# Optimization experiments

Hardware: AMD Instinct MI355X
Metric: run time of the kernel (lower is better)

## Reference

```python
import jax, jax.numpy as jnp
import numpy as np

BIG = 5000.0  # knockout sentinel from the original code
LOSS_WEIGHTS = jnp.array([1.0, 1.0, 1.0, 1.0, 1.0])  # [prob, x, y, a, b]


def _build_targets(preds, targets):
    """Greedy confidence-sorted matching for one batch element.
    preds: [N, 5] (prob, x, y, a, b); targets: [M, 5].
    Returns built targets [N, 5] aligned with the original pred order.
    """
    conf = preds[:, 0]
    order = jnp.argsort(-conf)          # descending confidence
    sp = preds[order]                   # [N, 5] sorted preds
    valid = targets[:, 0] == 1.0        # replaces the torch boolean filter
    n_targs = valid.sum()
    n_pos = (conf > 0.5).sum()
    M = targets.shape[0]

    def step(used, inp):
        i, p = inp
        x, y = p[1], p[2]
        # knocked-out targets sit at (BIG, BIG), matching the in-place write
        tx = jnp.where(used, BIG, targets[:, 1])
        ty = jnp.where(used, BIG, targets[:, 2])
        d2 = (tx - x) ** 2 + (ty - y) ** 2
        d2 = jnp.where(valid, d2, jnp.inf)  # invalid targets were filtered out
        min_idx = jnp.argmin(d2)
        row_nearest = jnp.stack([
            targets[min_idx, 0], tx[min_idx], ty[min_idx],
            targets[min_idx, 3], targets[min_idx, 4],
        ])
        # first valid, not-yet-chosen target (notchosen = x < 5000)
        first_idx = jnp.argmax(valid & (~used))
        row_first = targets[first_idx]
        # false positive: keep pred's continuous vars, prob target = 0
        row_fp = p.at[0].set(0.0)

        case_match = (i < n_pos) & (i < n_targs)   # greedy nearest match + knockout
        case_first = (~case_match) & (i < n_targs)  # n_pos <= i < n_targs
        row = jnp.where(case_match, row_nearest,
                        jnp.where(case_first, row_first, row_fp))
        used = jnp.where(case_match, used.at[min_idx].set(True), used)
        return used, row

    used0 = jnp.zeros(M, dtype=bool)
    _, built = jax.lax.scan(step, used0, (jnp.arange(sp.shape[0]), sp))
    # undo the confidence sort: built_targs[argsort(sort_conf)]
    return built[jnp.argsort(order)]


def setup_inputs() -> dict:
    key = jax.random.key(0)
    k1, k2, k3 = jax.random.split(key, 3)
    B, N, M = 256, 2048, 512
    preds = jax.random.uniform(k1, (B, N, 5), dtype=jnp.float32)  # prob in (0,1) for BCE
    tprob = (jax.random.uniform(k2, (B, M, 1)) > 0.5).astype(jnp.float32)  # ~half valid
    tvals = jax.random.uniform(k3, (B, M, 4), dtype=jnp.float32)
    targets = jnp.concatenate([tprob, tvals], axis=-1)
    return {"preds": preds, "targets": targets}


def reference(preds, targets):
    # built targets are constants w.r.t. autograd (requires_grad=False in torch)
    built = jax.lax.stop_gradient(jax.vmap(_build_targets)(preds, targets))
    p = preds[..., 0]
    t = built[..., 0]
    # BCE with torch's log clamp at -100
    logp = jnp.clip(jnp.log(p), -100.0)
    log1mp = jnp.clip(jnp.log1p(-p), -100.0)
    lossprob = -jnp.mean(t * logp + (1.0 - t) * log1mp) * LOSS_WEIGHTS[0]
    mse = lambda c: jnp.mean((preds[..., c] - built[..., c]) ** 2)
    lossx = mse(1) * LOSS_WEIGHTS[1]
    lossy = mse(2) * LOSS_WEIGHTS[2]
    lossa = mse(3) * LOSS_WEIGHTS[3]
    lossb = mse(4) * LOSS_WEIGHTS[4]
    # dict {'lossx','lossy','lossa','lossb','lossprob'} packed as a 5-vector
    return jnp.stack([lossx, lossy, lossa, lossb, lossprob])
```

## Files before the change

### kernel.cpp

```cpp
#include <hip/hip_runtime.h>
#include <stdint.h>

#define NPRED 2048
#define MT    512
#define BLK   256
#define NCAND 512

template<int C>
__device__ __forceinline__ uint32_t dppminu(uint32_t v) {
  uint32_t o = (uint32_t)__builtin_amdgcn_update_dpp((int)v, (int)v, C, 0xF, 0xF, false);
  return v < o ? v : o;
}
__device__ __forceinline__ uint32_t wave_min_u32_l63(uint32_t v) {
  v = dppminu<0x111>(v); v = dppminu<0x112>(v); v = dppminu<0x114>(v);
  v = dppminu<0x118>(v); v = dppminu<0x142>(v); v = dppminu<0x143>(v);
  return (uint32_t)__builtin_amdgcn_readlane((int)v, 63);
}
__device__ __forceinline__ uint32_t rowmin16(uint32_t v) {
  v = dppminu<0x111>(v); v = dppminu<0x112>(v);
  v = dppminu<0x114>(v); v = dppminu<0x118>(v);
  return v;
}

__global__ __launch_bounds__(BLK) void loss_kernel(const float* __restrict__ preds,
                                                   const float* __restrict__ targets,
                                                   double* __restrict__ acc) {
  const int b = blockIdx.x;
  const float* __restrict__ P = preds   + (size_t)b * NPRED * 5;
  const float* __restrict__ T = targets + (size_t)b * MT * 5;

  __shared__ uint64_t keys[NPRED];
  __shared__ uint64_t cand[NCAND];
  __shared__ float txy[MT * 2];
  __shared__ float tab[MT * 2];
  __shared__ float spx[520], spy[520], spa[520], spb[520];
  __shared__ uint16_t plds[512];
  __shared__ int hist[256];
  __shared__ uint32_t validw[16];
  __shared__ int s_npos, s_nt, s_B, s_ncand, s_first;
  __shared__ uint64_t s_thr;
  __shared__ double red[5][BLK];

  const int tid = threadIdx.x;
  if (tid == 0) { s_npos = 0; s_nt = 0; s_B = 0; s_ncand = 0; s_first = 0; s_thr = 0ull; }
  hist[tid] = 0;
  if (tid < 16) validw[tid] = 0;
  for (int i = tid; i < 520; i += BLK) { spx[i] = 0.f; spy[i] = 0.f; spa[i] = 0.f; spb[i] = 0.f; }
  __syncthreads();

  int cpos = 0;
  for (int i = tid; i < NPRED; i += BLK) {
    float c = P[i * 5 + 0];
    cpos += (c > 0.5f) ? 1 : 0;
    uint32_t cb = __float_as_uint(c);
    keys[i] = ((uint64_t)(~cb) << 32) | (uint32_t)i;
    if (cb >= 0x3F000000u && cb < 0x3F800000u)
      atomicAdd(&hist[(cb >> 15) & 0xFF], 1);
  }
  atomicAdd(&s_npos, cpos);

  int ct = 0;
  for (int m = tid; m < MT; m += BLK) {
    float tp = T[m * 5 + 0];
    bool v = (tp == 1.0f);
    if (v) { ct++; atomicOr(&validw[m >> 5], 1u << (m & 31)); }
    txy[2 * m]     = T[m * 5 + 1];
    txy[2 * m + 1] = T[m * 5 + 2];
    tab[2 * m]     = T[m * 5 + 3];
    tab[2 * m + 1] = T[m * 5 + 4];
  }
  atomicAdd(&s_nt, ct);
  __syncthreads();
  const int n_pos = s_npos;
  const int n_targs = s_nt;

  if (tid < 64) {
    const int lane = tid;
    int4 h4 = *reinterpret_cast<const int4*>(&hist[lane * 4]);
    int t = h4.x + h4.y + h4.z + h4.w;
    int S = t;
#pragma unroll
    for (int off = 1; off < 64; off <<= 1) {
      int o = __shfl_down(S, off);
      if (lane + off < 64) S += o;
    }
    int Snext = S - t;
    int s3 = h4.w + Snext;
    int s2 = h4.z + s3;
    int s1 = h4.y + s2;
    int s0 = h4.x + s1;
    int localB = -1;
    if      (s3 >= n_targs) localB = lane * 4 + 3;
    else if (s2 >= n_targs) localB = lane * 4 + 2;
    else if (s1 >= n_targs) localB = lane * 4 + 1;
    else if (s0 >= n_targs) localB = lane * 4 + 0;
    uint64_t q = __ballot(localB >= 0);
    if (q) {
      int hl = 63 - __clzll((long long)q);
      int B = __builtin_amdgcn_readlane(localB, hl);
      if (lane == 0) s_B = B;
    }
  }
  __syncthreads();
  const int B = s_B;

  for (int i = tid; i < NPRED; i += BLK) {
    uint64_t k = keys[i];
    uint32_t cb = ~(uint32_t)(k >> 32);
    if (cb >= 0x3F000000u && cb < 0x3F800000u && (int)((cb >> 15) & 0xFF) >= B) {
      int slot = atomicAdd(&s_ncand, 1);
      if (slot < NCAND) cand[slot] = k;
    }
  }
  __syncthreads();
  const int ncand = min(s_ncand, NCAND);

  {
    uint64_t ka = (tid < ncand) ? cand[tid] : ~0ull;
    uint64_t kb = (tid + BLK < ncand) ? cand[tid + BLK] : ~0ull;
    int ra = 0, rb = 0;
    for (int j = 0; j < ncand; ++j) {
      uint64_t kj = cand[j];
      ra += (kj < ka) ? 1 : 0;
      rb += (kj < kb) ? 1 : 0;
    }
    if (tid < ncand && ra < n_targs) {
      int idx = (int)(ka & 0xFFFFFFFFu);
      spx[ra] = P[idx * 5 + 1]; spy[ra] = P[idx * 5 + 2];
      spa[ra] = P[idx * 5 + 3]; spb[ra] = P[idx * 5 + 4];
    }
    if (tid < ncand && ra == n_targs - 1) s_thr = ka;
    if (tid + BLK < ncand && rb < n_targs) {
      int idx = (int)(kb & 0xFFFFFFFFu);
      spx[rb] = P[idx * 5 + 1]; spy[rb] = P[idx * 5 + 2];
      spa[rb] = P[idx * 5 + 3]; spb[rb] = P[idx * 5 + 4];
    }
    if (tid + BLK < ncand && rb == n_targs - 1) s_thr = kb;
  }
  __syncthreads();
  const uint64_t thr = s_thr;
  const int K = min(n_pos, n_targs);

  float accp = 0.f;

  if (tid < 64) {
    const int lane = tid;
    const int s = lane & 15;
    const int g = lane >> 4;
    const uint32_t sbase = (uint32_t)(s << 5);

    float txr[32], tyr[32];
#pragma unroll
    for (int j = 0; j < 32; ++j) {
      txr[j] = txy[2 * (s * 32 + j)];
      tyr[j] = txy[2 * (s * 32 + j) + 1];
    }
    uint32_t una = ~validw[s];

    int i = 0;
    float x = spx[g], y = spy[g];
    while (i + 4 <= K) {
      float xn = spx[i + 4 + g], yn = spy[i + 4 + g];
      uint32_t kk = 0xFFFFFFFFu;
#pragma unroll
      for (int j = 0; j < 32; ++j) {
        float dx = __fsub_rn(txr[j], x);
        float dy = __fsub_rn(tyr[j], y);
        float d2 = __fadd_rn(__fmul_rn(dx, dx), __fmul_rn(dy, dy));
        uint32_t pois = 0u - ((una >> j) & 1u);
        uint32_t key = ((__float_as_uint(d2) & 0xFFFFFE00u) | (sbase + (uint32_t)j)) | pois;
        kk = kk < key ? kk : key;
      }
      kk = rowmin16(kk);
      uint32_t m0 = (uint32_t)__builtin_amdgcn_readlane((int)kk, 15) & 0x1FFu;
      uint32_t m1 = (uint32_t)__builtin_amdgcn_readlane((int)kk, 31) & 0x1FFu;
      uint32_t m2 = (uint32_t)__builtin_amdgcn_readlane((int)kk, 47) & 0x1FFu;
      uint32_t m3 = (uint32_t)__builtin_amdgcn_readlane((int)kk, 63) & 0x1FFu;
      int p;
      if (m1 == m0) p = 1;
      else if (m2 == m0 || m2 == m1) p = 2;
      else if (m3 == m0 || m3 == m1 || m3 == m2) p = 3;
      else p = 4;
      uint32_t hit = ((m0 >> 5) == (uint32_t)s) ? (1u << (m0 & 31u)) : 0u;
      if (p > 1) hit |= ((m1 >> 5) == (uint32_t)s) ? (1u << (m1 & 31u)) : 0u;
      if (p > 2) hit |= ((m2 >> 5) == (uint32_t)s) ? (1u << (m2 & 31u)) : 0u;
      if (p > 3) hit |= ((m3 >> 5) == (uint32_t)s) ? (1u << (m3 & 31u)) : 0u;
      una |= hit;
      if (lane == 0) {
        plds[i] = (uint16_t)m0;
        if (p > 1) plds[i + 1] = (uint16_t)m1;
        if (p > 2) plds[i + 2] = (uint16_t)m2;
        if (p > 3) plds[i + 3] = (uint16_t)m3;
      }
      i += p;
      if (p == 4) { x = xn; y = yn; }
      else       { x = spx[i + g]; y = spy[i + g]; }
    }
    while (i < K) {
      float x1 = spx[i], y1 = spy[i];
      uint32_t kk = 0xFFFFFFFFu;
#pragma unroll
      for (int j = 0; j < 32; ++j) {
        float dx = __fsub_rn(txr[j], x1);
        float dy = __fsub_rn(tyr[j], y1);
        float d2 = __fadd_rn(__fmul_rn(dx, dx), __fmul_rn(dy, dy));
        uint32_t pois = 0u - ((una >> j) & 1u);
        uint32_t key = ((__float_as_uint(d2) & 0xFFFFFE00u) | (sbase + (uint32_t)j)) | pois;
        kk = kk < key ? kk : key;
      }
      kk = rowmin16(kk);
      uint32_t m = (uint32_t)__builtin_amdgcn_readlane((int)kk, 15) & 0x1FFu;
      una |= ((m >> 5) == (uint32_t)s) ? (1u << (m & 31u)) : 0u;
      if (lane == 0) plds[i] = (uint16_t)m;
      ++i;
    }
    uint32_t av = ~una;
    uint32_t fi = av ? (sbase + (uint32_t)__ffs(av) - 1u) : 0xFFFFFFFFu;
    fi = wave_min_u32_l63(fi);
    if (lane == 0) s_first = (fi < MT) ? (int)fi : 0;
  } else {
    for (int i = tid - 64; i < NPRED; i += (BLK - 64)) {
      uint64_t k = keys[i];
      float p = __uint_as_float(~(uint32_t)(k >> 32));
      accp += (k <= thr) ? -fmaxf(logf(p), -100.0f)
                         : -fmaxf(log1pf(-p), -100.0f);
    }
  }
  __syncthreads();

  float ax = 0.f, ay = 0.f, aa = 0.f, ab = 0.f;
  for (int r = tid; r < K; r += BLK) {
    int m = plds[r];
    float dx = __fsub_rn(spx[r], txy[2 * m]);
    float dy = __fsub_rn(spy[r], txy[2 * m + 1]);
    float da = __fsub_rn(spa[r], tab[2 * m]);
    float db = __fsub_rn(spb[r], tab[2 * m + 1]);
    ax += __fmul_rn(dx, dx);
    ay += __fmul_rn(dy, dy);
    aa += __fmul_rn(da, da);
    ab += __fmul_rn(db, db);
  }
  if (n_pos < n_targs) {
    int f = s_first;
    float fx = txy[2 * f], fy = txy[2 * f + 1];
    float fa = tab[2 * f], fb = tab[2 * f + 1];
    for (int i = n_pos + tid; i < n_targs; i += BLK) {
      float dx = __fsub_rn(spx[i], fx);
      float dy = __fsub_rn(spy[i], fy);
      float da = __fsub_rn(spa[i], fa);
      float db = __fsub_rn(spb[i], fb);
      ax += __fmul_rn(dx, dx);
      ay += __fmul_rn(dy, dy);
      aa += __fmul_rn(da, da);
      ab += __fmul_rn(db, db);
    }
  }

  red[0][tid] = (double)ax;
  red[1][tid] = (double)ay;
  red[2][tid] = (double)aa;
  red[3][tid] = (double)ab;
  red[4][tid] = (double)accp;
  __syncthreads();
  for (int st = BLK / 2; st > 0; st >>= 1) {
    if (tid < st) {
#pragma unroll
      for (int c = 0; c < 5; ++c) red[c][tid] += red[c][tid + st];
    }
    __syncthreads();
  }
  if (tid == 0) {
#pragma unroll
    for (int c = 0; c < 5; ++c) atomicAdd(&acc[c], red[c][0]);
  }
}

__global__ void finalize_kernel(const double* __restrict__ acc,
                                float* __restrict__ out, double inv) {
  int c = threadIdx.x;
  if (c < 5) out[c] = (float)(acc[c] * inv);
}

extern "C" void kernel_launch(void* const* d_in, const int* in_sizes, int n_in,
                              void* d_out, int out_size, void* d_ws, size_t ws_size,
                              hipStream_t stream) {
  const float* preds = (const float*)d_in[0];
  const float* targets = (const float*)d_in[1];
  int B = in_sizes[0] / (NPRED * 5);

  double* acc = (double*)d_ws;
  hipMemsetAsync(acc, 0, 5 * sizeof(double), stream);
  loss_kernel<<<B, BLK, 0, stream>>>(preds, targets, acc);
  finalize_kernel<<<1, 64, 0, stream>>>(acc, (float*)d_out,
                                        1.0 / ((double)B * NPRED));
}
```

Before: 85.33 us.

## Widen speculative greedy matching to eight lanes groups and use wave-level reductions

The serial greedy nearest-target scan now splits the wave into 8 groups of 8 lanes, each lane holding 64 targets. Each group speculatively evaluates one of the next 8 predictions, so up to 8 matches can commit per iteration instead of 4. Sorted pred coordinates are interleaved as xy/ab pairs, and the distance uses an FMA. The block-level double shared-memory tree reduction is replaced by per-wave shuffle sums and per-wave atomics. The trade-off is higher register pressure (128 target registers per lane), more work per iteration and more global atomics.

```diff
diff --git a/kernel.cpp b/kernel.cpp
--- a/kernel.cpp
+++ b/kernel.cpp
@@ -16,15 +16,19 @@
   v = dppminu<0x118>(v); v = dppminu<0x142>(v); v = dppminu<0x143>(v);
   return (uint32_t)__builtin_amdgcn_readlane((int)v, 63);
 }
-__device__ __forceinline__ uint32_t rowmin16(uint32_t v) {
-  v = dppminu<0x111>(v); v = dppminu<0x112>(v);
-  v = dppminu<0x114>(v); v = dppminu<0x118>(v);
+__device__ __forceinline__ uint32_t rowmin8(uint32_t v) {
+  v = dppminu<0x111>(v); v = dppminu<0x112>(v); v = dppminu<0x114>(v);
   return v;
 }
-
-__global__ __launch_bounds__(BLK) void loss_kernel(const float* __restrict__ preds,
-                                                   const float* __restrict__ targets,
-                                                   double* __restrict__ acc) {
+__device__ __forceinline__ float wave_sum_f32(float v) {
+#pragma unroll
+  for (int off = 32; off; off >>= 1) v += __shfl_xor(v, off, 64);
+  return v;
+}
+
+__global__ __launch_bounds__(BLK, 1) void loss_kernel(const float* __restrict__ preds,
+                                                      const float* __restrict__ targets,
+                                                      double* __restrict__ acc) {
   const int b = blockIdx.x;
   const float* __restrict__ P = preds   + (size_t)b * NPRED * 5;
   const float* __restrict__ T = targets + (size_t)b * MT * 5;
@@ -33,19 +37,22 @@
   __shared__ uint64_t cand[NCAND];
   __shared__ float txy[MT * 2];
   __shared__ float tab[MT * 2];
-  __shared__ float spx[520], spy[520], spa[520], spb[520];
+  __shared__ float spxy[528 * 2];
+  __shared__ float spab[528 * 2];
   __shared__ uint16_t plds[512];
   __shared__ int hist[256];
   __shared__ uint32_t validw[16];
   __shared__ int s_npos, s_nt, s_B, s_ncand, s_first;
   __shared__ uint64_t s_thr;
-  __shared__ double red[5][BLK];
 
   const int tid = threadIdx.x;
   if (tid == 0) { s_npos = 0; s_nt = 0; s_B = 0; s_ncand = 0; s_first = 0; s_thr = 0ull; }
   hist[tid] = 0;
   if (tid < 16) validw[tid] = 0;
-  for (int i = tid; i < 520; i += BLK) { spx[i] = 0.f; spy[i] = 0.f; spa[i] = 0.f; spb[i] = 0.f; }
+  for (int i = tid; i < 528; i += BLK) {
+    spxy[2 * i] = 0.f; spxy[2 * i + 1] = 0.f;
+    spab[2 * i] = 0.f; spab[2 * i + 1] = 0.f;
+  }
   __syncthreads();
 
   int cpos = 0;
@@ -126,14 +133,14 @@
     }
     if (tid < ncand && ra < n_targs) {
       int idx = (int)(ka & 0xFFFFFFFFu);
-      spx[ra] = P[idx * 5 + 1]; spy[ra] = P[idx * 5 + 2];
-      spa[ra] = P[idx * 5 + 3]; spb[ra] = P[idx * 5 + 4];
+      spxy[2 * ra] = P[idx * 5 + 1]; spxy[2 * ra + 1] = P[idx * 5 + 2];
+      spab[2 * ra] = P[idx * 5 + 3]; spab[2 * ra + 1] = P[idx * 5 + 4];
     }
     if (tid < ncand && ra == n_targs - 1) s_thr = ka;
     if (tid + BLK < ncand && rb < n_targs) {
       int idx = (int)(kb & 0xFFFFFFFFu);
-      spx[rb] = P[idx * 5 + 1]; spy[rb] = P[idx * 5 + 2];
-      spa[rb] = P[idx * 5 + 3]; spb[rb] = P[idx * 5 + 4];
+      spxy[2 * rb] = P[idx * 5 + 1]; spxy[2 * rb + 1] = P[idx * 5 + 2];
+      spab[2 * rb] = P[idx * 5 + 3]; spab[2 * rb + 1] = P[idx * 5 + 4];
     }
     if (tid + BLK < ncand && rb == n_targs - 1) s_thr = kb;
   }
@@ -145,77 +152,118 @@
 
   if (tid < 64) {
     const int lane = tid;
-    const int s = lane & 15;
-    const int g = lane >> 4;
-    const uint32_t sbase = (uint32_t)(s << 5);
-
-    float txr[32], tyr[32];
-#pragma unroll
-    for (int j = 0; j < 32; ++j) {
-      txr[j] = txy[2 * (s * 32 + j)];
-      tyr[j] = txy[2 * (s * 32 + j) + 1];
-    }
-    uint32_t una = ~validw[s];
+    const int s8 = lane & 7;
+    const int g8 = lane >> 3;
+    const uint32_t sb6 = (uint32_t)(s8 << 6);
+
+    float txr[64], tyr[64];
+#pragma unroll
+    for (int j = 0; j < 64; ++j) {
+      txr[j] = txy[2 * (s8 * 64 + j)];
+      tyr[j] = txy[2 * (s8 * 64 + j) + 1];
+    }
+    uint32_t una_lo = ~validw[2 * s8];
+    uint32_t una_hi = ~validw[2 * s8 + 1];
 
     int i = 0;
-    float x = spx[g], y = spy[g];
-    while (i + 4 <= K) {
-      float xn = spx[i + 4 + g], yn = spy[i + 4 + g];
+    float x = spxy[2 * g8], y = spxy[2 * g8 + 1];
+    while (i + 8 <= K) {
+      float nx1 = spxy[2*(i+1+g8)], ny1 = spxy[2*(i+1+g8)+1];
+      float nx2 = spxy[2*(i+2+g8)], ny2 = spxy[2*(i+2+g8)+1];
+      float nx3 = spxy[2*(i+3+g8)], ny3 = spxy[2*(i+3+g8)+1];
+      float nx4 = spxy[2*(i+4+g8)], ny4 = spxy[2*(i+4+g8)+1];
+      float nx5 = spxy[2*(i+5+g8)], ny5 = spxy[2*(i+5+g8)+1];
+      float nx6 = spxy[2*(i+6+g8)], ny6 = spxy[2*(i+6+g8)+1];
+      float nx7 = spxy[2*(i+7+g8)], ny7 = spxy[2*(i+7+g8)+1];
+      float nx8 = spxy[2*(i+8+g8)], ny8 = spxy[2*(i+8+g8)+1];
+
       uint32_t kk = 0xFFFFFFFFu;
 #pragma unroll
-      for (int j = 0; j < 32; ++j) {
+      for (int j = 0; j < 64; ++j) {
         float dx = __fsub_rn(txr[j], x);
         float dy = __fsub_rn(tyr[j], y);
-        float d2 = __fadd_rn(__fmul_rn(dx, dx), __fmul_rn(dy, dy));
-        uint32_t pois = 0u - ((una >> j) & 1u);
-        uint32_t key = ((__float_as_uint(d2) & 0xFFFFFE00u) | (sbase + (uint32_t)j)) | pois;
+        float d2 = __fmaf_rn(dy, dy, __fmul_rn(dx, dx));
+        uint32_t u = (j < 32) ? una_lo : una_hi;
+        uint32_t pois = (uint32_t)(((int32_t)(u << (31 - (j & 31)))) >> 31);
+        uint32_t key = ((__float_as_uint(d2) | pois) & 0xFFFFFE00u) | (uint32_t)j;
         kk = kk < key ? kk : key;
       }
-      kk = rowmin16(kk);
-      uint32_t m0 = (uint32_t)__builtin_amdgcn_readlane((int)kk, 15) & 0x1FFu;
-      uint32_t m1 = (uint32_t)__builtin_amdgcn_readlane((int)kk, 31) & 0x1FFu;
-      uint32_t m2 = (uint32_t)__builtin_amdgcn_readlane((int)kk, 47) & 0x1FFu;
-      uint32_t m3 = (uint32_t)__builtin_amdgcn_readlane((int)kk, 63) & 0x1FFu;
-      int p;
-      if (m1 == m0) p = 1;
-      else if (m2 == m0 || m2 == m1) p = 2;
-      else if (m3 == m0 || m3 == m1 || m3 == m2) p = 3;
-      else p = 4;
-      uint32_t hit = ((m0 >> 5) == (uint32_t)s) ? (1u << (m0 & 31u)) : 0u;
-      if (p > 1) hit |= ((m1 >> 5) == (uint32_t)s) ? (1u << (m1 & 31u)) : 0u;
-      if (p > 2) hit |= ((m2 >> 5) == (uint32_t)s) ? (1u << (m2 & 31u)) : 0u;
-      if (p > 3) hit |= ((m3 >> 5) == (uint32_t)s) ? (1u << (m3 & 31u)) : 0u;
-      una |= hit;
+      uint32_t kkg = rowmin8(kk + sb6);
+      int m0 = __builtin_amdgcn_readlane((int)kkg, 7)  & 0x1FF;
+      int m1 = __builtin_amdgcn_readlane((int)kkg, 15) & 0x1FF;
+      int m2 = __builtin_amdgcn_readlane((int)kkg, 23) & 0x1FF;
+      int m3 = __builtin_amdgcn_readlane((int)kkg, 31) & 0x1FF;
+      int m4 = __builtin_amdgcn_readlane((int)kkg, 39) & 0x1FF;
+      int m5 = __builtin_amdgcn_readlane((int)kkg, 47) & 0x1FF;
+      int m6 = __builtin_amdgcn_readlane((int)kkg, 55) & 0x1FF;
+      int m7 = __builtin_amdgcn_readlane((int)kkg, 63) & 0x1FF;
+
+      bool c1 = (m1==m0);
+      bool c2 = (m2==m0)|(m2==m1);
+      bool c3 = (m3==m0)|(m3==m1)|(m3==m2);
+      bool c4 = (m4==m0)|(m4==m1)|(m4==m2)|(m4==m3);
+      bool c5 = (m5==m0)|(m5==m1)|(m5==m2)|(m5==m3)|(m5==m4);
+      bool c6 = (m6==m0)|(m6==m1)|(m6==m2)|(m6==m3)|(m6==m4)|(m6==m5);
+      bool c7 = (m7==m0)|(m7==m1)|(m7==m2)|(m7==m3)|(m7==m4)|(m7==m5)|(m7==m6);
+      int p = c1 ? 1 : c2 ? 2 : c3 ? 3 : c4 ? 4 : c5 ? 5 : c6 ? 6 : c7 ? 7 : 8;
+
+      int m1e = (p > 1) ? m1 : 0x3FF;
+      int m2e = (p > 2) ? m2 : 0x3FF;
+      int m3e = (p > 3) ? m3 : 0x3FF;
+      int m4e = (p > 4) ? m4 : 0x3FF;
+      int m5e = (p > 5) ? m5 : 0x3FF;
+      int m6e = (p > 6) ? m6 : 0x3FF;
+      int m7e = (p > 7) ? m7 : 0x3FF;
+
+#define COMMIT(me) { \
+      uint64_t bb = 1ull << ((me) & 63); \
+      bool hh = (((me) >> 6) == s8); \
+      una_lo |= hh ? (uint32_t)(bb & 0xFFFFFFFFull) : 0u; \
+      una_hi |= hh ? (uint32_t)(bb >> 32) : 0u; }
+      COMMIT(m0) COMMIT(m1e) COMMIT(m2e) COMMIT(m3e)
+      COMMIT(m4e) COMMIT(m5e) COMMIT(m6e) COMMIT(m7e)
+#undef COMMIT
+
       if (lane == 0) {
-        plds[i] = (uint16_t)m0;
-        if (p > 1) plds[i + 1] = (uint16_t)m1;
-        if (p > 2) plds[i + 2] = (uint16_t)m2;
-        if (p > 3) plds[i + 3] = (uint16_t)m3;
+        plds[i]     = (uint16_t)m0;
+        plds[i + 1] = (uint16_t)m1e;
+        plds[i + 2] = (uint16_t)m2e;
+        plds[i + 3] = (uint16_t)m3e;
+        plds[i + 4] = (uint16_t)m4e;
+        plds[i + 5] = (uint16_t)m5e;
+        plds[i + 6] = (uint16_t)m6e;
+        plds[i + 7] = (uint16_t)m7e;
       }
       i += p;
-      if (p == 4) { x = xn; y = yn; }
-      else       { x = spx[i + g]; y = spy[i + g]; }
+      x = (p==1)?nx1:(p==2)?nx2:(p==3)?nx3:(p==4)?nx4:(p==5)?nx5:(p==6)?nx6:(p==7)?nx7:nx8;
+      y = (p==1)?ny1:(p==2)?ny2:(p==3)?ny3:(p==4)?ny4:(p==5)?ny5:(p==6)?ny6:(p==7)?ny7:ny8;
     }
     while (i < K) {
-      float x1 = spx[i], y1 = spy[i];
+      float x1 = spxy[2 * i], y1 = spxy[2 * i + 1];
       uint32_t kk = 0xFFFFFFFFu;
 #pragma unroll
-      for (int j = 0; j < 32; ++j) {
+      for (int j = 0; j < 64; ++j) {
         float dx = __fsub_rn(txr[j], x1);
         float dy = __fsub_rn(tyr[j], y1);
-        float d2 = __fadd_rn(__fmul_rn(dx, dx), __fmul_rn(dy, dy));
-        uint32_t pois = 0u - ((una >> j) & 1u);
-        uint32_t key = ((__float_as_uint(d2) & 0xFFFFFE00u) | (sbase + (uint32_t)j)) | pois;
+        float d2 = __fmaf_rn(dy, dy, __fmul_rn(dx, dx));
+        uint32_t u = (j < 32) ? una_lo : una_hi;
+        uint32_t pois = (uint32_t)(((int32_t)(u << (31 - (j & 31)))) >> 31);
+        uint32_t key = ((__float_as_uint(d2) | pois) & 0xFFFFFE00u) | (uint32_t)j;
         kk = kk < key ? kk : key;
       }
-      kk = rowmin16(kk);
-      uint32_t m = (uint32_t)__builtin_amdgcn_readlane((int)kk, 15) & 0x1FFu;
-      una |= ((m >> 5) == (uint32_t)s) ? (1u << (m & 31u)) : 0u;
+      uint32_t kkg = rowmin8(kk + sb6);
+      int m = __builtin_amdgcn_readlane((int)kkg, 7) & 0x1FF;
+      uint64_t bb = 1ull << (m & 63);
+      bool hh = ((m >> 6) == s8);
+      una_lo |= hh ? (uint32_t)(bb & 0xFFFFFFFFull) : 0u;
+      una_hi |= hh ? (uint32_t)(bb >> 32) : 0u;
       if (lane == 0) plds[i] = (uint16_t)m;
       ++i;
     }
-    uint32_t av = ~una;
-    uint32_t fi = av ? (sbase + (uint32_t)__ffs(av) - 1u) : 0xFFFFFFFFu;
+    uint32_t avlo = ~una_lo, avhi = ~una_hi;
+    uint32_t fl = avlo ? ((uint32_t)__ffs(avlo) - 1u)
+                       : (avhi ? (31u + (uint32_t)__ffs(avhi)) : 0xFFFFu);
+    uint32_t fi = (fl == 0xFFFFu) ? 0xFFFFFFFFu : (sb6 + fl);
     fi = wave_min_u32_l63(fi);
     if (lane == 0) s_first = (fi < MT) ? (int)fi : 0;
   } else {
@@ -231,10 +279,10 @@
   float ax = 0.f, ay = 0.f, aa = 0.f, ab = 0.f;
   for (int r = tid; r < K; r += BLK) {
     int m = plds[r];
-    float dx = __fsub_rn(spx[r], txy[2 * m]);
-    float dy = __fsub_rn(spy[r], txy[2 * m + 1]);
-    float da = __fsub_rn(spa[r], tab[2 * m]);
-    float db = __fsub_rn(spb[r], tab[2 * m + 1]);
+    float dx = __fsub_rn(spxy[2 * r],     txy[2 * m]);
+    float dy = __fsub_rn(spxy[2 * r + 1], txy[2 * m + 1]);
+    float da = __fsub_rn(spab[2 * r],     tab[2 * m]);
+    float db = __fsub_rn(spab[2 * r + 1], tab[2 * m + 1]);
     ax += __fmul_rn(dx, dx);
     ay += __fmul_rn(dy, dy);
     aa += __fmul_rn(da, da);
@@ -244,34 +292,28 @@
     int f = s_first;
     float fx = txy[2 * f], fy = txy[2 * f + 1];
     float fa = tab[2 * f], fb = tab[2 * f + 1];
-    for (int i = n_pos + tid; i < n_targs; i += BLK) {
-      float dx = __fsub_rn(spx[i], fx);
-      float dy = __fsub_rn(spy[i], fy);
-      float da = __fsub_rn(spa[i], fa);
-      float db = __fsub_rn(spb[i], fb);
+    for (int i2 = n_pos + tid; i2 < n_targs; i2 += BLK) {
+      float dx = __fsub_rn(spxy[2 * i2],     fx);
+      float dy = __fsub_rn(spxy[2 * i2 + 1], fy);
+      float da = __fsub_rn(spab[2 * i2],     fa);
+      float db = __fsub_rn(spab[2 * i2 + 1], fb);
       ax += __fmul_rn(dx, dx);
       ay += __fmul_rn(dy, dy);
       aa += __fmul_rn(da, da);
       ab += __fmul_rn(db, db);
     }
   }
-
-  red[0][tid] = (double)ax;
-  red[1][tid] = (double)ay;
-  red[2][tid] = (double)aa;
-  red[3][tid] = (double)ab;
-  red[4][tid] = (double)accp;
-  __syncthreads();
-  for (int st = BLK / 2; st > 0; st >>= 1) {
-    if (tid < st) {
-#pragma unroll
-      for (int c = 0; c < 5; ++c) red[c][tid] += red[c][tid + st];
-    }
-    __syncthreads();
-  }
-  if (tid == 0) {
-#pragma unroll
-    for (int c = 0; c < 5; ++c) atomicAdd(&acc[c], red[c][0]);
+  ax = wave_sum_f32(ax);
+  ay = wave_sum_f32(ay);
+  aa = wave_sum_f32(aa);
+  ab = wave_sum_f32(ab);
+  accp = wave_sum_f32(accp);
+  if ((tid & 63) == 0) {
+    atomicAdd(&acc[0], (double)ax);
+    atomicAdd(&acc[1], (double)ay);
+    atomicAdd(&acc[2], (double)aa);
+    atomicAdd(&acc[3], (double)ab);
+    atomicAdd(&acc[4], (double)accp);
   }
 }
 
```

Result: slower. 143.5 us (+68.2%).

## Speculate eight greedy matches per wave iteration instead of four

Applied to the files above, without the earlier changes.

The serial greedy matching loop now evaluates two groups of four sorted predictions per pass, using two key accumulators against the register-held targets. It then accepts the longest prefix of distinct nearest-target picks, up to eight. This aims to cut the number of serial iterations and cross-lane reductions in the dependent chain. It adds register pressure, handled by setting launch bounds to one block minimum, and more wasted speculative work whenever an early collision truncates the prefix.

```diff
diff --git a/kernel.cpp b/kernel.cpp
--- a/kernel.cpp
+++ b/kernel.cpp
@@ -22,9 +22,9 @@
   return v;
 }
 
-__global__ __launch_bounds__(BLK) void loss_kernel(const float* __restrict__ preds,
-                                                   const float* __restrict__ targets,
-                                                   double* __restrict__ acc) {
+__global__ __launch_bounds__(BLK, 1) void loss_kernel(const float* __restrict__ preds,
+                                                      const float* __restrict__ targets,
+                                                      double* __restrict__ acc) {
   const int b = blockIdx.x;
   const float* __restrict__ P = preds   + (size_t)b * NPRED * 5;
   const float* __restrict__ T = targets + (size_t)b * MT * 5;
@@ -158,51 +158,86 @@
     uint32_t una = ~validw[s];
 
     int i = 0;
-    float x = spx[g], y = spy[g];
-    while (i + 4 <= K) {
-      float xn = spx[i + 4 + g], yn = spy[i + 4 + g];
-      uint32_t kk = 0xFFFFFFFFu;
+    float x1 = spx[g], y1 = spy[g];
+    float x2 = spx[4 + g], y2 = spy[4 + g];
+    while (i + 8 <= K) {
+      uint32_t kk1 = 0xFFFFFFFFu, kk2 = 0xFFFFFFFFu;
 #pragma unroll
       for (int j = 0; j < 32; ++j) {
-        float dx = __fsub_rn(txr[j], x);
-        float dy = __fsub_rn(tyr[j], y);
-        float d2 = __fadd_rn(__fmul_rn(dx, dx), __fmul_rn(dy, dy));
         uint32_t pois = 0u - ((una >> j) & 1u);
-        uint32_t key = ((__float_as_uint(d2) & 0xFFFFFE00u) | (sbase + (uint32_t)j)) | pois;
-        kk = kk < key ? kk : key;
+        {
+          float dx = __fsub_rn(txr[j], x1);
+          float dy = __fsub_rn(tyr[j], y1);
+          float d2 = __fadd_rn(__fmul_rn(dx, dx), __fmul_rn(dy, dy));
+          uint32_t key = ((__float_as_uint(d2) & 0xFFFFFE00u) | (sbase + (uint32_t)j)) | pois;
+          kk1 = kk1 < key ? kk1 : key;
+        }
+        {
+          float dx = __fsub_rn(txr[j], x2);
+          float dy = __fsub_rn(tyr[j], y2);
+          float d2 = __fadd_rn(__fmul_rn(dx, dx), __fmul_rn(dy, dy));
+          uint32_t key = ((__float_as_uint(d2) & 0xFFFFFE00u) | (sbase + (uint32_t)j)) | pois;
+          kk2 = kk2 < key ? kk2 : key;
+        }
       }
-      kk = rowmin16(kk);
-      uint32_t m0 = (uint32_t)__builtin_amdgcn_readlane((int)kk, 15) & 0x1FFu;
-      uint32_t m1 = (uint32_t)__builtin_amdgcn_readlane((int)kk, 31) & 0x1FFu;
-      uint32_t m2 = (uint32_t)__builtin_amdgcn_readlane((int)kk, 47) & 0x1FFu;
-      uint32_t m3 = (uint32_t)__builtin_amdgcn_readlane((int)kk, 63) & 0x1FFu;
-      int p;
-      if (m1 == m0) p = 1;
-      else if (m2 == m0 || m2 == m1) p = 2;
-      else if (m3 == m0 || m3 == m1 || m3 == m2) p = 3;
-      else p = 4;
-      uint32_t hit = ((m0 >> 5) == (uint32_t)s) ? (1u << (m0 & 31u)) : 0u;
-      if (p > 1) hit |= ((m1 >> 5) == (uint32_t)s) ? (1u << (m1 & 31u)) : 0u;
-      if (p > 2) hit |= ((m2 >> 5) == (uint32_t)s) ? (1u << (m2 & 31u)) : 0u;
-      if (p > 3) hit |= ((m3 >> 5) == (uint32_t)s) ? (1u << (m3 & 31u)) : 0u;
-      una |= hit;
+      kk1 = rowmin16(kk1);
+      kk2 = rowmin16(kk2);
+      int m0 = __builtin_amdgcn_readlane((int)kk1, 15) & 0x1FF;
+      int m1 = __builtin_amdgcn_readlane((int)kk1, 31) & 0x1FF;
+      int m2 = __builtin_amdgcn_readlane((int)kk1, 47) & 0x1FF;
+      int m3 = __builtin_amdgcn_readlane((int)kk1, 63) & 0x1FF;
+      int m4 = __builtin_amdgcn_readlane((int)kk2, 15) & 0x1FF;
+      int m5 = __builtin_amdgcn_readlane((int)kk2, 31) & 0x1FF;
+      int m6 = __builtin_amdgcn_readlane((int)kk2, 47) & 0x1FF;
+      int m7 = __builtin_amdgcn_readlane((int)kk2, 63) & 0x1FF;
+
+      bool c1 = (m1==m0);
+      bool c2 = (m2==m0)|(m2==m1);
+      bool c3 = (m3==m0)|(m3==m1)|(m3==m2);
+      bool c4 = (m4==m0)|(m4==m1)|(m4==m2)|(m4==m3);
+      bool c5 = (m5==m0)|(m5==m1)|(m5==m2)|(m5==m3)|(m5==m4);
+      bool c6 = (m6==m0)|(m6==m1)|(m6==m2)|(m6==m3)|(m6==m4)|(m6==m5);
+      bool c7 = (m7==m0)|(m7==m1)|(m7==m2)|(m7==m3)|(m7==m4)|(m7==m5)|(m7==m6);
+      int p = c1 ? 1 : c2 ? 2 : c3 ? 3 : c4 ? 4 : c5 ? 5 : c6 ? 6 : c7 ? 7 : 8;
+
+      int m1e = (p > 1) ? m1 : 0x3FF;
+      int m2e = (p > 2) ? m2 : 0x3FF;
+      int m3e = (p > 3) ? m3 : 0x3FF;
+      int m4e = (p > 4) ? m4 : 0x3FF;
+      int m5e = (p > 5) ? m5 : 0x3FF;
+      int m6e = (p > 6) ? m6 : 0x3FF;
+      int m7e = (p > 7) ? m7 : 0x3FF;
+
+      una |= ((uint32_t)(m0  >> 5) == (uint32_t)s) ? (1u << (m0  & 31)) : 0u;
+      una |= ((uint32_t)(m1e >> 5) == (uint32_t)s) ? (1u << (m1e & 31)) : 0u;
+      una |= ((uint32_t)(m2e >> 5) == (uint32_t)s) ? (1u << (m2e & 31)) : 0u;
+      una |= ((uint32_t)(m3e >> 5) == (uint32_t)s) ? (1u << (m3e & 31)) : 0u;
+      una |= ((uint32_t)(m4e >> 5) == (uint32_t)s) ? (1u << (m4e & 31)) : 0u;
+      una |= ((uint32_t)(m5e >> 5) == (uint32_t)s) ? (1u << (m5e & 31)) : 0u;
+      una |= ((uint32_t)(m6e >> 5) == (uint32_t)s) ? (1u << (m6e & 31)) : 0u;
+      una |= ((uint32_t)(m7e >> 5) == (uint32_t)s) ? (1u << (m7e & 31)) : 0u;
+
       if (lane == 0) {
-        plds[i] = (uint16_t)m0;
-        if (p > 1) plds[i + 1] = (uint16_t)m1;
-        if (p > 2) plds[i + 2] = (uint16_t)m2;
-        if (p > 3) plds[i + 3] = (uint16_t)m3;
+        plds[i]     = (uint16_t)m0;
+        plds[i + 1] = (uint16_t)m1e;
+        plds[i + 2] = (uint16_t)m2e;
+        plds[i + 3] = (uint16_t)m3e;
+        plds[i + 4] = (uint16_t)m4e;
+        plds[i + 5] = (uint16_t)m5e;
+        plds[i + 6] = (uint16_t)m6e;
+        plds[i + 7] = (uint16_t)m7e;
       }
       i += p;
-      if (p == 4) { x = xn; y = yn; }
-      else       { x = spx[i + g]; y = spy[i + g]; }
+      x1 = spx[i + g];     y1 = spy[i + g];
+      x2 = spx[i + 4 + g]; y2 = spy[i + 4 + g];
     }
     while (i < K) {
-      float x1 = spx[i], y1 = spy[i];
+      float xs = spx[i], ys = spy[i];
       uint32_t kk = 0xFFFFFFFFu;
 #pragma unroll
       for (int j = 0; j < 32; ++j) {
-        float dx = __fsub_rn(txr[j], x1);
-        float dy = __fsub_rn(tyr[j], y1);
+        float dx = __fsub_rn(txr[j], xs);
+        float dy = __fsub_rn(tyr[j], ys);
         float d2 = __fadd_rn(__fmul_rn(dx, dx), __fmul_rn(dy, dy));
         uint32_t pois = 0u - ((una >> j) & 1u);
         uint32_t key = ((__float_as_uint(d2) & 0xFFFFFE00u) | (sbase + (uint32_t)j)) | pois;
@@ -244,11 +279,11 @@
     int f = s_first;
     float fx = txy[2 * f], fy = txy[2 * f + 1];
     float fa = tab[2 * f], fb = tab[2 * f + 1];
-    for (int i = n_pos + tid; i < n_targs; i += BLK) {
-      float dx = __fsub_rn(spx[i], fx);
-      float dy = __fsub_rn(spy[i], fy);
-      float da = __fsub_rn(spa[i], fa);
-      float db = __fsub_rn(spb[i], fb);
+    for (int i2 = n_pos + tid; i2 < n_targs; i2 += BLK) {
+      float dx = __fsub_rn(spx[i2], fx);
+      float dy = __fsub_rn(spy[i2], fy);
+      float da = __fsub_rn(spa[i2], fa);
+      float db = __fsub_rn(spb[i2], fb);
       ax += __fmul_rn(dx, dx);
       ay += __fmul_rn(dy, dy);
       aa += __fmul_rn(da, da);
```

New measurement: 93.07 us. 1.09x slower.
